# Optimization experiments

Hardware: AMD Instinct MI355X
Metric: run time of the kernel (lower is better)

Reference implementation:

```python
import jax, jax.numpy as jnp
import numpy as np

B, T, D_IN, D_H, D_OUT = 64, 512, 1024, 1024, 1024

def setup_inputs() -> dict:
    key = jax.random.key(0)
    k1, k2, k3 = jax.random.split(key, 3)
    scale_h = 1.0 / np.sqrt(D_IN + D_H)
    return {
        "input": jax.random.normal(k1, (B, T, D_IN), dtype=jnp.float32),
        "hidden": jnp.zeros((B, D_H), dtype=jnp.float32),
        "W_h": jax.random.normal(k2, (D_H, D_IN + D_H), dtype=jnp.float32) * scale_h,
        "b_h": jnp.zeros((D_H,), dtype=jnp.float32),
        "W_o": jax.random.normal(k3, (D_OUT, D_IN + D_H), dtype=jnp.float32) * scale_h,
        "b_o": jnp.zeros((D_OUT,), dtype=jnp.float32),
    }

def reference(input, hidden, W_h, b_h, W_o, b_o):
    # input: [B, T, D_in]; hidden: [B, D_h]
    # per step: combined = [x_t, h]; h' = combined @ W_h^T + b_h; o = combined @ W_o^T + b_o
    xs = jnp.swapaxes(input, 0, 1)  # [T, B, D_in]

    def step(h, x_t):
        combined = jnp.concatenate([x_t, h], axis=1)  # [B, D_in + D_h]
        h_new = combined @ W_h.T + b_h                # [B, D_h]
        o = combined @ W_o.T + b_o                    # [B, D_out]
        return h_new, o

    _, outs = jax.lax.scan(step, hidden, xs)          # outs: [T, B, D_out]
    return jnp.swapaxes(outs, 0, 1)                   # [B, T, D_out]
```

## Files before the change

### kernel.cpp

```cpp
#include <hip/hip_runtime.h>
#include <hip/hip_bf16.h>


typedef _Float16 f16;
typedef _Float16 f16x8 __attribute__((ext_vector_type(8)));
typedef _Float16 f16x4 __attribute__((ext_vector_type(4)));
typedef float f32x4 __attribute__((ext_vector_type(4)));
typedef int i32x4 __attribute__((ext_vector_type(4)));

#define T_LEN 512
#define BATCH 64
#define M_TOT (BATCH * T_LEN)


__global__ void k_prep_w(const float* __restrict__ Wh, const float* __restrict__ Wo,
                         f16* __restrict__ Wx, f16* __restrict__ Wr) {
    int n = blockIdx.x;
    int t4 = threadIdx.x * 4;
    const float* src = (n < 1024) ? (Wh + (size_t)n * 2048)
                                  : (Wo + (size_t)(n - 1024) * 2048);
    float4 a = *reinterpret_cast<const float4*>(src + t4);
    float4 b = *reinterpret_cast<const float4*>(src + 1024 + t4);
    f16x4 va, vb;
    va[0]=(f16)a.x; va[1]=(f16)a.y; va[2]=(f16)a.z; va[3]=(f16)a.w;
    vb[0]=(f16)b.x; vb[1]=(f16)b.y; vb[2]=(f16)b.z; vb[3]=(f16)b.w;
    *reinterpret_cast<f16x4*>(Wx + (size_t)n*1024 + t4) = va;
    *reinterpret_cast<f16x4*>(Wr + (size_t)n*1024 + t4) = vb;
}

__global__ void k_prep_x(const float* __restrict__ X, f16* __restrict__ Xf) {
    size_t i = ((size_t)blockIdx.x * 256 + threadIdx.x) * 8;
    float4 a = *reinterpret_cast<const float4*>(X + i);
    float4 b = *reinterpret_cast<const float4*>(X + i + 4);
    f16x8 v;
    v[0]=(f16)a.x; v[1]=(f16)a.y; v[2]=(f16)a.z; v[3]=(f16)a.w;
    v[4]=(f16)b.x; v[5]=(f16)b.y; v[6]=(f16)b.z; v[7]=(f16)b.w;
    *reinterpret_cast<f16x8*>(Xf + i) = v;
}

__global__ void k_init_h(const float* __restrict__ H0, f16* __restrict__ Hs) {
    int tid = blockIdx.x * 256 + threadIdx.x;
    int b = tid >> 7, kb = tid & 127;
    float4 x0 = *reinterpret_cast<const float4*>(H0 + (size_t)b*1024 + kb*8);
    float4 x1 = *reinterpret_cast<const float4*>(H0 + (size_t)b*1024 + kb*8 + 4);
    f16x8 v;
    v[0]=(f16)x0.x; v[1]=(f16)x0.y; v[2]=(f16)x0.z; v[3]=(f16)x0.w;
    v[4]=(f16)x1.x; v[5]=(f16)x1.y; v[6]=(f16)x1.z; v[7]=(f16)x1.w;
    size_t idx = (size_t)(b >> 4)*16384 + (size_t)kb*128 + (size_t)(b & 15)*8;
    *reinterpret_cast<f16x8*>(Hs + idx) = v;
}

__global__ void k_zero_flags(unsigned int* __restrict__ flags) {
    flags[blockIdx.x * 256 + threadIdx.x] = 0;
}

__global__ __launch_bounds__(256) void k_gemm1(
    const f16* __restrict__ Af, const f16* __restrict__ Bm,
    const float* __restrict__ bh, const float* __restrict__ bo,
    f16* __restrict__ Xh, float* __restrict__ Out)
{
    __shared__ f16 As[128*32];
    __shared__ f16 Bs[128*32];
    int m0 = blockIdx.x * 128;
    int n0 = blockIdx.y * 128;
    int t = threadIdx.x;
    int l = t & 63, w = t >> 6;
    int wm = w >> 1, wn = w & 1;
    int lm = l & 15, lh = l >> 4;

    f32x4 acc[4][4];
    #pragma unroll
    for (int i = 0; i < 4; i++)
        #pragma unroll
        for (int j = 0; j < 4; j++) acc[i][j] = (f32x4){0.f,0.f,0.f,0.f};

    const size_t lgo = (size_t)(l >> 2) * 2048 + (size_t)(l & 3) * 16;

    for (int kt = 0; kt < 32; ++kt) {
        __syncthreads();
        {
            const char* ga = (const char*)(Af + (size_t)(m0 + w*32) * 1024 + kt*32);
            const char* gb = (const char*)(Bm + (size_t)(n0 + w*32) * 1024 + kt*32);
            char* la = (char*)As + w * 2048;
            char* lb = (char*)Bs + w * 2048;
            #pragma unroll
            for (int j = 0; j < 2; ++j) {
                __builtin_amdgcn_global_load_lds(
                    (const __attribute__((address_space(1))) void*)(ga + (size_t)j*32768 + lgo),
                    (__attribute__((address_space(3))) void*)(la + j*1024), 16, 0, 0);
                __builtin_amdgcn_global_load_lds(
                    (const __attribute__((address_space(1))) void*)(gb + (size_t)j*32768 + lgo),
                    (__attribute__((address_space(3))) void*)(lb + j*1024), 16, 0, 0);
            }
        }
        asm volatile("s_waitcnt vmcnt(0)" ::: "memory");
        __syncthreads();

        f16x8 af[4], bf[4];
        #pragma unroll
        for (int i = 0; i < 4; i++)
            af[i] = *reinterpret_cast<const f16x8*>(As + (64*wm + 16*i + lm)*32 + 8*lh);
        #pragma unroll
        for (int j = 0; j < 4; j++)
            bf[j] = *reinterpret_cast<const f16x8*>(Bs + (64*wn + 16*j + lm)*32 + 8*lh);
        #pragma unroll
        for (int i = 0; i < 4; i++)
            #pragma unroll
            for (int j = 0; j < 4; j++)
                acc[i][j] = __builtin_amdgcn_mfma_f32_16x16x32_f16(af[i], bf[j], acc[i][j], 0, 0, 0);
    }

    int r0 = lh * 4;
    bool isH = (n0 < 1024);
    #pragma unroll
    for (int i = 0; i < 4; i++)
        #pragma unroll
        for (int j = 0; j < 4; j++) {
            int gmb = m0 + 64*wm + 16*i + r0;
            int gn  = n0 + 64*wn + 16*j + lm;
            #pragma unroll
            for (int r = 0; r < 4; r++) {
                float v = acc[i][j][r];
                int gm = gmb + r;
                if (isH) {
                    int tt = gm & 511, bb = gm >> 9;
                    size_t idx = (size_t)tt*65536 + (size_t)(bb>>4)*16384
                               + (size_t)(gn>>3)*128 + (size_t)(bb&15)*8 + (gn&7);
                    Xh[idx] = (f16)(v + bh[gn]);
                } else {
                    Out[(size_t)gm*1024 + (gn - 1024)] = v + bo[gn - 1024];
                }
            }
        }
}

__global__ __launch_bounds__(256) void k_sq(const f16* __restrict__ P, f16* __restrict__ Pout)
{
    __shared__ f16 As[128][40];
    __shared__ f16 Bs[128][40];
    int m0 = blockIdx.x * 128, n0 = blockIdx.y * 128;
    int t = threadIdx.x;
    int l = t & 63, wid = t >> 6;
    int wm = wid >> 1, wn = wid & 1;
    int lm = l & 15, lh = l >> 4;

    f32x4 acc[4][4];
    #pragma unroll
    for (int i = 0; i < 4; i++)
        #pragma unroll
        for (int j = 0; j < 4; j++) acc[i][j] = (f32x4){0.f,0.f,0.f,0.f};

    for (int kt = 0; kt < 32; ++kt) {
        __syncthreads();
        #pragma unroll
        for (int c = t; c < 512; c += 256) {
            int row = c >> 2, q = c & 3;
            *reinterpret_cast<float4*>(&As[row][q*8]) =
                *reinterpret_cast<const float4*>(P + (size_t)(m0+row)*1024 + kt*32 + q*8);
        }
        #pragma unroll
        for (int c = t; c < 512; c += 256) {
            int r = c >> 4, q = c & 15;
            f16x8 v = *reinterpret_cast<const f16x8*>(P + (size_t)(kt*32 + r)*1024 + n0 + q*8);
            #pragma unroll
            for (int e = 0; e < 8; ++e) Bs[q*8+e][r] = v[e];
        }
        __syncthreads();

        f16x8 af[4], bf[4];
        #pragma unroll
        for (int i = 0; i < 4; i++)
            af[i] = *reinterpret_cast<const f16x8*>(&As[64*wm + 16*i + lm][8*lh]);
        #pragma unroll
        for (int j = 0; j < 4; j++)
            bf[j] = *reinterpret_cast<const f16x8*>(&Bs[64*wn + 16*j + lm][8*lh]);
        #pragma unroll
        for (int i = 0; i < 4; i++)
            #pragma unroll
            for (int j = 0; j < 4; j++)
                acc[i][j] = __builtin_amdgcn_mfma_f32_16x16x32_f16(af[i], bf[j], acc[i][j], 0, 0, 0);
    }

    int r0 = lh * 4;
    #pragma unroll
    for (int i = 0; i < 4; i++)
        #pragma unroll
        for (int j = 0; j < 4; j++) {
            int gmb = m0 + 64*wm + 16*i + r0;
            int gn  = n0 + 64*wn + 16*j + lm;
            #pragma unroll
            for (int r = 0; r < 4; r++)
                Pout[(size_t)(gmb+r)*1024 + gn] = (f16)acc[i][j][r];
        }
}

__global__ __launch_bounds__(256) void k_vlevel(
    const f16* __restrict__ M, const f16* __restrict__ Src, f16* __restrict__ Dst,
    int srcOff, int srcStep, int dstOff, int dstStep)
{
    __shared__ f16 As[4096];
    __shared__ f16 Bs[128*32];
    int m0 = blockIdx.x * 128;
    int n0 = blockIdx.y * 128;
    int t = threadIdx.x;
    int l = t & 63, w = t >> 6;
    int wm = w >> 1, wn = w & 1;
    int lm = l & 15, lh = l >> 4;

    f32x4 acc[4][4];
    #pragma unroll
    for (int i = 0; i < 4; i++)
        #pragma unroll
        for (int j = 0; j < 4; j++) acc[i][j] = (f32x4){0.f,0.f,0.f,0.f};

    const size_t lgo = (size_t)(l >> 2) * 2048 + (size_t)(l & 3) * 16;
    const int kd0 = m0 >> 6;

    for (int kt = 0; kt < 32; ++kt) {
        __syncthreads();
        {
            #pragma unroll
            for (int j = 0; j < 2; ++j) {
                int ch  = w*2 + j;
                int kdl = ch >> 2, bgc = ch & 3;
                size_t slab = (size_t)(srcOff + srcStep * (2*(kd0 + kdl)));
                const char* gsrc = (const char*)(Src + slab*65536
                                    + (size_t)bgc*16384 + (size_t)kt*512) + (size_t)l*16;
                __builtin_amdgcn_global_load_lds(
                    (const __attribute__((address_space(1))) void*)gsrc,
                    (__attribute__((address_space(3))) void*)((char*)As + ch*1024), 16, 0, 0);
            }
            const char* gb = (const char*)(M + (size_t)(n0 + w*32) * 1024 + kt*32);
            char* lb = (char*)Bs + w * 2048;
            #pragma unroll
            for (int j = 0; j < 2; ++j)
                __builtin_amdgcn_global_load_lds(
                    (const __attribute__((address_space(1))) void*)(gb + (size_t)j*32768 + lgo),
                    (__attribute__((address_space(3))) void*)(lb + j*1024), 16, 0, 0);
        }
        asm volatile("s_waitcnt vmcnt(0)" ::: "memory");
        __syncthreads();

        f16x8 af[4], bf[4];
        #pragma unroll
        for (int i = 0; i < 4; i++)
            af[i] = *reinterpret_cast<const f16x8*>(As + wm*2048 + i*512 + lh*128 + lm*8);
        #pragma unroll
        for (int j = 0; j < 4; j++)
            bf[j] = *reinterpret_cast<const f16x8*>(Bs + (64*wn + 16*j + lm)*32 + 8*lh);
        #pragma unroll
        for (int i = 0; i < 4; i++)
            #pragma unroll
            for (int j = 0; j < 4; j++)
                acc[i][j] = __builtin_amdgcn_mfma_f32_16x16x32_f16(af[i], bf[j], acc[i][j], 0, 0, 0);
    }

    int r0 = lh * 4;
    #pragma unroll
    for (int i = 0; i < 4; i++)
        #pragma unroll
        for (int j = 0; j < 4; j++) {
            int gmb = m0 + 64*wm + 16*i + r0;
            int gn  = n0 + 64*wn + 16*j + lm;
            #pragma unroll
            for (int r = 0; r < 4; r++) {
                int gm = gmb + r;
                int kd = gm >> 6, bb = gm & 63;
                size_t pidx = (size_t)(bb>>4)*16384 + (size_t)(gn>>3)*128
                            + (size_t)(bb&15)*8 + (gn&7);
                size_t aslab = (size_t)(srcOff + srcStep * (2*kd + 1));
                float add = (float)Src[aslab*65536 + pidx];
                size_t dslab = (size_t)(dstOff + dstStep * kd);
                Dst[dslab*65536 + pidx] = (f16)(acc[i][j][r] + add);
            }
        }
}

__global__ void __launch_bounds__(256) __attribute__((amdgpu_waves_per_eu(1, 1)))
k_chain(
    const f16* __restrict__ W,
    const f16* __restrict__ U,
    f16* __restrict__ Hs,
    unsigned int* __restrict__ flags,
    int nstep, int mode, int nch)
{
    int wg = blockIdx.x;
    int r_ = wg & 7, s_ = wg >> 3;
    int g, cg, p, bg;
    if (mode == 1) { g = r_ >> 1; cg = ((r_ & 1) << 3) | s_; p = 0;       bg = g;     }
    else           { g = 2*r_ + (s_ >> 4); cg = s_ & 15;     p = g >> 2;  bg = g & 3; }
    int w  = threadIdx.x >> 6;
    int l  = threadIdx.x & 63;
    int lm = l & 15, lh = l >> 4;
    int ccol = cg * 64 + w * 16 + lm;

    __shared__ f16 hbuf[16384];
    __shared__ float lt[4][16][17];

    f16x8 bw[32];
    #pragma unroll
    for (int kt = 0; kt < 32; ++kt)
        bw[kt] = *reinterpret_cast<const f16x8*>(W + (size_t)ccol * 1024 + kt*32 + lh*8);
    #pragma unroll
    for (int kt = 0; kt < 32; ++kt)
        asm volatile("" : "+v"(bw[kt]));

    const int flagBase = g * 16;
    int b_ep = l & 15, cb_ep = l >> 4;

    for (int t = 0; t < nstep; ++t) {
        if (t > 0) {
            if (threadIdx.x < 16) {
                unsigned int tgt = (unsigned int)t;
                const unsigned int* fp = &flags[(flagBase + (int)threadIdx.x) * 8];
                while (__hip_atomic_load(fp, __ATOMIC_RELAXED, __HIP_MEMORY_SCOPE_AGENT) < tgt)
                    __builtin_amdgcn_s_sleep(1);
            }
            __syncthreads();
            asm volatile("" ::: "memory");
        }

        for (int i = 0; i < nch; ++i) {
            int c = p * nch + i;
            size_t rSlab, wSlab, uSlab;
            if (mode == 1) { rSlab = (size_t)(16*t); wSlab = rSlab + 16; uSlab = rSlab + 8; }
            else           { rSlab = (size_t)(c*16 + t); wSlab = rSlab + 1; uSlab = rSlab; }

            if (i > 0) __syncthreads();

            f16x8 xv;
            int cblk = cg*8 + w*2 + cb_ep;
            if (l < 32)
                xv = *reinterpret_cast<const f16x8*>(
                    U + uSlab*65536 + (size_t)bg*16384 + (size_t)cblk*128 + b_ep*8);

            {
                const char* gsrc = (const char*)Hs + (rSlab*65536 + (size_t)bg*16384)*2
                                 + (size_t)w*8192 + (size_t)l*16;
                char* ldst = (char*)hbuf + (size_t)w*8192;
                #pragma unroll
                for (int q = 0; q < 8; ++q)
                    __builtin_amdgcn_global_load_lds(
                        (const __attribute__((address_space(1))) void*)(gsrc + q*1024),
                        (__attribute__((address_space(3))) void*)(ldst + q*1024),
                        16, 0, 0);
            }
            asm volatile("s_waitcnt vmcnt(0)" ::: "memory");
            __syncthreads();

            f32x4 a0 = (f32x4){0.f,0.f,0.f,0.f};
            f32x4 a1 = (f32x4){0.f,0.f,0.f,0.f};
            #pragma unroll
            for (int kt = 0; kt < 32; ++kt) {
                f16x8 af = *reinterpret_cast<const f16x8*>(&hbuf[(size_t)(kt*4 + lh)*128 + lm*8]);
                if (kt & 1) a1 = __builtin_amdgcn_mfma_f32_16x16x32_f16(af, bw[kt], a1, 0, 0, 0);
                else        a0 = __builtin_amdgcn_mfma_f32_16x16x32_f16(af, bw[kt], a0, 0, 0, 0);
            }
            f32x4 acc = a0 + a1;

            #pragma unroll
            for (int r = 0; r < 4; ++r)
                lt[w][lh*4 + r][lm] = acc[r];

            if (l < 32) {
                f16x8 hv;
                #pragma unroll
                for (int e = 0; e < 8; ++e)
                    hv[e] = (f16)(lt[w][b_ep][cb_ep*8 + e] + (float)xv[e]);
                f16* dst = Hs + wSlab*65536 + (size_t)bg*16384 + (size_t)cblk*128 + b_ep*8;
                i32x4 iv = __builtin_bit_cast(i32x4, hv);
                asm volatile("global_store_dwordx4 %0, %1, off sc0 sc1"
                             :: "v"(dst), "v"(iv) : "memory");
            }
        }

        asm volatile("s_waitcnt vmcnt(0)" ::: "memory");
        __syncthreads();
        if (threadIdx.x == 0) {
            __builtin_amdgcn_fence(__ATOMIC_RELEASE, "agent");
            __hip_atomic_store(&flags[(flagBase + cg)*8], (unsigned int)(t+1),
                               __ATOMIC_RELAXED, __HIP_MEMORY_SCOPE_AGENT);
        }
    }
}

__global__ __launch_bounds__(256) void k_gemm2(
    const f16* __restrict__ Hs, const f16* __restrict__ Bm, float* __restrict__ Out)
{
    __shared__ f16 As[4096];
    __shared__ f16 Bs[128*32];
    int m0 = blockIdx.x * 128;
    int n0 = blockIdx.y * 128;
    int t = threadIdx.x;
    int l = t & 63, w = t >> 6;
    int wm = w >> 1, wn = w & 1;
    int lm = l & 15, lh = l >> 4;

    f32x4 acc[4][4];
    #pragma unroll
    for (int i = 0; i < 4; i++)
        #pragma unroll
        for (int j = 0; j < 4; j++) acc[i][j] = (f32x4){0.f,0.f,0.f,0.f};

    const size_t lgo = (size_t)(l >> 2) * 2048 + (size_t)(l & 3) * 16;
    const int tt0 = m0 >> 6;

    for (int kt = 0; kt < 32; ++kt) {
        __syncthreads();
        {
            #pragma unroll
            for (int j = 0; j < 2; ++j) {
                int ch  = w*2 + j;
                int ttl = ch >> 2, bgc = ch & 3;
                const char* gsrc = (const char*)(Hs + (size_t)(tt0 + ttl)*65536
                                    + (size_t)bgc*16384 + (size_t)kt*512) + (size_t)l*16;
                __builtin_amdgcn_global_load_lds(
                    (const __attribute__((address_space(1))) void*)gsrc,
                    (__attribute__((address_space(3))) void*)((char*)As + ch*1024), 16, 0, 0);
            }
            const char* gb = (const char*)(Bm + (size_t)(n0 + w*32) * 1024 + kt*32);
            char* lb = (char*)Bs + w * 2048;
            #pragma unroll
            for (int j = 0; j < 2; ++j)
                __builtin_amdgcn_global_load_lds(
                    (const __attribute__((address_space(1))) void*)(gb + (size_t)j*32768 + lgo),
                    (__attribute__((address_space(3))) void*)(lb + j*1024), 16, 0, 0);
        }
        asm volatile("s_waitcnt vmcnt(0)" ::: "memory");
        __syncthreads();

        f16x8 af[4], bf[4];
        #pragma unroll
        for (int i = 0; i < 4; i++)
            af[i] = *reinterpret_cast<const f16x8*>(As + wm*2048 + i*512 + lh*128 + lm*8);
        #pragma unroll
        for (int j = 0; j < 4; j++)
            bf[j] = *reinterpret_cast<const f16x8*>(Bs + (64*wn + 16*j + lm)*32 + 8*lh);
        #pragma unroll
        for (int i = 0; i < 4; i++)
            #pragma unroll
            for (int j = 0; j < 4; j++)
                acc[i][j] = __builtin_amdgcn_mfma_f32_16x16x32_f16(af[i], bf[j], acc[i][j], 0, 0, 0);
    }

    int r0 = lh * 4;
    #pragma unroll
    for (int i = 0; i < 4; i++)
        #pragma unroll
        for (int j = 0; j < 4; j++) {
            int gmb = m0 + 64*wm + 16*i + r0;
            int gn  = n0 + 64*wn + 16*j + lm;
            #pragma unroll
            for (int r = 0; r < 4; r++) {
                int gm = gmb + r;
                int bb = gm & 63, tt = gm >> 6;
                size_t o = ((size_t)bb*512 + tt)*1024 + gn;
                Out[o] += acc[i][j][r];
            }
        }
}


extern "C" void kernel_launch(void* const* d_in, const int* in_sizes, int n_in,
                              void* d_out, int out_size, void* d_ws, size_t ws_size,
                              hipStream_t stream) {
    const float* X  = (const float*)d_in[0];
    const float* H0 = (const float*)d_in[1];
    const float* Wh = (const float*)d_in[2];
    const float* bh = (const float*)d_in[3];
    const float* Wo = (const float*)d_in[4];
    const float* bo = (const float*)d_in[5];
    float* Out = (float*)d_out;

    char* ws = (char*)d_ws;
    f16* Wx = (f16*)(ws);
    f16* Pa = (f16*)(ws);
    f16* Pb = (f16*)(ws + (size_t)2*1024*1024);
    f16* Wr = (f16*)(ws + (size_t)4*1024*1024);
    f16* Xh = (f16*)(ws + (size_t)8*1024*1024);
    f16* Hs = (f16*)(ws + (size_t)8*1024*1024 + (size_t)M_TOT*1024*2);
    f16* Xf = Hs;
    unsigned int* flags = (unsigned int*)(ws + (size_t)8*1024*1024 + (size_t)2*M_TOT*1024*2);

    hipLaunchKernelGGL(k_prep_w, dim3(2048), dim3(256), 0, stream, Wh, Wo, Wx, Wr);
    hipLaunchKernelGGL(k_prep_x, dim3(16384), dim3(256), 0, stream, X, Xf);
    hipLaunchKernelGGL(k_gemm1, dim3(256, 16), dim3(256), 0, stream, Xf, Wx, bh, bo, Xh, Out);
    hipLaunchKernelGGL(k_init_h, dim3(32), dim3(256), 0, stream, H0, Hs);

    hipLaunchKernelGGL(k_sq, dim3(8,8), dim3(256), 0, stream, Wr, Pa);
    hipLaunchKernelGGL(k_vlevel, dim3(128,8), dim3(256), 0, stream, Wr, Xh, Hs, 0,1, 1,1);
    hipLaunchKernelGGL(k_vlevel, dim3(64,8),  dim3(256), 0, stream, Pa, Hs, Hs, 1,1, 257,2);
    hipLaunchKernelGGL(k_sq, dim3(8,8), dim3(256), 0, stream, Pa, Pb);
    hipLaunchKernelGGL(k_vlevel, dim3(32,8),  dim3(256), 0, stream, Pb, Hs, Hs, 257,2, 2,4);
    hipLaunchKernelGGL(k_sq, dim3(8,8), dim3(256), 0, stream, Pb, Pa);
    hipLaunchKernelGGL(k_vlevel, dim3(16,8),  dim3(256), 0, stream, Pa, Hs, Hs, 2,4, 8,16);
    hipLaunchKernelGGL(k_sq, dim3(8,8), dim3(256), 0, stream, Pa, Pb);

    hipLaunchKernelGGL(k_zero_flags, dim3(8), dim3(256), 0, stream, flags);
    {
        int nstep = 31, mode = 1, nch = 1;
        void* args[] = { (void*)&Pb, (void*)&Hs, (void*)&Hs, (void*)&flags,
                         (void*)&nstep, (void*)&mode, (void*)&nch };
        if (hipLaunchCooperativeKernel((const void*)k_chain, dim3(64), dim3(256),
                                       args, 0, stream) != hipSuccess) {
            hipLaunchKernelGGL(k_chain, dim3(64), dim3(256), 0, stream,
                               Pb, Hs, Hs, flags, 31, 1, 1);
        }
    }

    hipLaunchKernelGGL(k_zero_flags, dim3(8), dim3(256), 0, stream, flags);
    {
        int nstep = 15, mode = 2, nch = 8;
        void* args[] = { (void*)&Wr, (void*)&Xh, (void*)&Hs, (void*)&flags,
                         (void*)&nstep, (void*)&mode, (void*)&nch };
        if (hipLaunchCooperativeKernel((const void*)k_chain, dim3(256), dim3(256),
                                       args, 0, stream) != hipSuccess) {
            hipLaunchKernelGGL(k_chain, dim3(256), dim3(256), 0, stream,
                               Wr, Xh, Hs, flags, 15, 2, 8);
        }
    }

    f16* Wro = Wr + (size_t)1024*1024;
    hipLaunchKernelGGL(k_gemm2, dim3(256, 8), dim3(256), 0, stream, Hs, Wro, Out);
}
```

Measured before the change: 1.107 ms.

## Double-buffer hidden-state staging in chain kernel and widen gemm1 K tile

The recurrent chain kernel now keeps two LDS buffers for the hidden state and issues the async global-to-LDS load for the next chunk before computing the current one. It waits only on the older loads via a partial vmcnt, so load latency overlaps the MFMA work. Separately, gemm1 stages 64-wide K tiles instead of 32, halving its loop iterations and barriers. The costs are double the LDS for hbuf, an extra barrier per chunk, and a vmcnt count that is hand-tuned and fragile. Mode 1 (nch=1 likely) sees no overlap.

```diff
diff --git a/kernel.cpp b/kernel.cpp
--- a/kernel.cpp
+++ b/kernel.cpp
@@ -59,8 +59,8 @@
     const float* __restrict__ bh, const float* __restrict__ bo,
     f16* __restrict__ Xh, float* __restrict__ Out)
 {
-    __shared__ f16 As[128*32];
-    __shared__ f16 Bs[128*32];
+    __shared__ f16 As[128*64];
+    __shared__ f16 Bs[128*64];
     int m0 = blockIdx.x * 128;
     int n0 = blockIdx.y * 128;
     int t = threadIdx.x;
@@ -74,40 +74,43 @@
         #pragma unroll
         for (int j = 0; j < 4; j++) acc[i][j] = (f32x4){0.f,0.f,0.f,0.f};
 
-    const size_t lgo = (size_t)(l >> 2) * 2048 + (size_t)(l & 3) * 16;
-
-    for (int kt = 0; kt < 32; ++kt) {
+    const size_t lgo = (size_t)(l >> 3) * 2048 + (size_t)(l & 7) * 16;
+
+    for (int kt = 0; kt < 16; ++kt) {
         __syncthreads();
         {
-            const char* ga = (const char*)(Af + (size_t)(m0 + w*32) * 1024 + kt*32);
-            const char* gb = (const char*)(Bm + (size_t)(n0 + w*32) * 1024 + kt*32);
-            char* la = (char*)As + w * 2048;
-            char* lb = (char*)Bs + w * 2048;
-            #pragma unroll
-            for (int j = 0; j < 2; ++j) {
-                __builtin_amdgcn_global_load_lds(
-                    (const __attribute__((address_space(1))) void*)(ga + (size_t)j*32768 + lgo),
+            const char* ga = (const char*)(Af + (size_t)(m0 + w*32) * 1024 + kt*64);
+            const char* gb = (const char*)(Bm + (size_t)(n0 + w*32) * 1024 + kt*64);
+            char* la = (char*)As + w * 4096;
+            char* lb = (char*)Bs + w * 4096;
+            #pragma unroll
+            for (int j = 0; j < 4; ++j) {
+                __builtin_amdgcn_global_load_lds(
+                    (const __attribute__((address_space(1))) void*)(ga + (size_t)j*16384 + lgo),
                     (__attribute__((address_space(3))) void*)(la + j*1024), 16, 0, 0);
                 __builtin_amdgcn_global_load_lds(
-                    (const __attribute__((address_space(1))) void*)(gb + (size_t)j*32768 + lgo),
+                    (const __attribute__((address_space(1))) void*)(gb + (size_t)j*16384 + lgo),
                     (__attribute__((address_space(3))) void*)(lb + j*1024), 16, 0, 0);
             }
         }
         asm volatile("s_waitcnt vmcnt(0)" ::: "memory");
         __syncthreads();
 
-        f16x8 af[4], bf[4];
-        #pragma unroll
-        for (int i = 0; i < 4; i++)
-            af[i] = *reinterpret_cast<const f16x8*>(As + (64*wm + 16*i + lm)*32 + 8*lh);
-        #pragma unroll
-        for (int j = 0; j < 4; j++)
-            bf[j] = *reinterpret_cast<const f16x8*>(Bs + (64*wn + 16*j + lm)*32 + 8*lh);
-        #pragma unroll
-        for (int i = 0; i < 4; i++)
+        #pragma unroll
+        for (int kh = 0; kh < 2; ++kh) {
+            f16x8 af[4], bf[4];
+            #pragma unroll
+            for (int i = 0; i < 4; i++)
+                af[i] = *reinterpret_cast<const f16x8*>(As + (64*wm + 16*i + lm)*64 + kh*32 + 8*lh);
             #pragma unroll
             for (int j = 0; j < 4; j++)
-                acc[i][j] = __builtin_amdgcn_mfma_f32_16x16x32_f16(af[i], bf[j], acc[i][j], 0, 0, 0);
+                bf[j] = *reinterpret_cast<const f16x8*>(Bs + (64*wn + 16*j + lm)*64 + kh*32 + 8*lh);
+            #pragma unroll
+            for (int i = 0; i < 4; i++)
+                #pragma unroll
+                for (int j = 0; j < 4; j++)
+                    acc[i][j] = __builtin_amdgcn_mfma_f32_16x16x32_f16(af[i], bf[j], acc[i][j], 0, 0, 0);
+        }
     }
 
     int r0 = lh * 4;
@@ -294,7 +297,7 @@
     int lm = l & 15, lh = l >> 4;
     int ccol = cg * 64 + w * 16 + lm;
 
-    __shared__ f16 hbuf[16384];
+    __shared__ f16 hbuf[2][16384];
     __shared__ float lt[4][16][17];
 
     f16x8 bw[32];
@@ -307,6 +310,7 @@
 
     const int flagBase = g * 16;
     int b_ep = l & 15, cb_ep = l >> 4;
+    int cblk = cg*8 + w*2 + cb_ep;
 
     for (int t = 0; t < nstep; ++t) {
         if (t > 0) {
@@ -320,39 +324,54 @@
             asm volatile("" ::: "memory");
         }
 
+        auto slabs = [&](int i, size_t& rS, size_t& wS, size_t& uS) {
+            if (mode == 1) { rS = (size_t)(16*t); wS = rS + 16; uS = rS + 8; }
+            else { int c = p*nch + i; rS = (size_t)(c*16 + t); wS = rS + 1; uS = rS; }
+        };
+        auto STAGE = [&](size_t rS, int buf) {
+            const char* gsrc = (const char*)Hs + (rS*65536 + (size_t)bg*16384)*2
+                             + (size_t)w*8192 + (size_t)l*16;
+            char* ldst = (char*)&hbuf[buf][0] + (size_t)w*8192;
+            #pragma unroll
+            for (int q = 0; q < 8; ++q)
+                __builtin_amdgcn_global_load_lds(
+                    (const __attribute__((address_space(1))) void*)(gsrc + q*1024),
+                    (__attribute__((address_space(3))) void*)(ldst + q*1024),
+                    16, 0, 0);
+        };
+        auto XV = [&](size_t uS) -> f16x8 {
+            f16x8 v = {};
+            if (l < 32)
+                v = *reinterpret_cast<const f16x8*>(
+                    U + uS*65536 + (size_t)bg*16384 + (size_t)cblk*128 + b_ep*8);
+            return v;
+        };
+
+        f16x8 xv0, xv1;
+        {
+            size_t rS, wS, uS; slabs(0, rS, wS, uS);
+            STAGE(rS, 0);
+            xv0 = XV(uS);
+        }
+
         for (int i = 0; i < nch; ++i) {
-            int c = p * nch + i;
-            size_t rSlab, wSlab, uSlab;
-            if (mode == 1) { rSlab = (size_t)(16*t); wSlab = rSlab + 16; uSlab = rSlab + 8; }
-            else           { rSlab = (size_t)(c*16 + t); wSlab = rSlab + 1; uSlab = rSlab; }
-
-            if (i > 0) __syncthreads();
-
-            f16x8 xv;
-            int cblk = cg*8 + w*2 + cb_ep;
-            if (l < 32)
-                xv = *reinterpret_cast<const f16x8*>(
-                    U + uSlab*65536 + (size_t)bg*16384 + (size_t)cblk*128 + b_ep*8);
-
-            {
-                const char* gsrc = (const char*)Hs + (rSlab*65536 + (size_t)bg*16384)*2
-                                 + (size_t)w*8192 + (size_t)l*16;
-                char* ldst = (char*)hbuf + (size_t)w*8192;
-                #pragma unroll
-                for (int q = 0; q < 8; ++q)
-                    __builtin_amdgcn_global_load_lds(
-                        (const __attribute__((address_space(1))) void*)(gsrc + q*1024),
-                        (__attribute__((address_space(3))) void*)(ldst + q*1024),
-                        16, 0, 0);
-            }
-            asm volatile("s_waitcnt vmcnt(0)" ::: "memory");
+            int nxt = i + 1;
+            if (nxt < nch) {
+                size_t rS, wS, uS; slabs(nxt, rS, wS, uS);
+                STAGE(rS, nxt & 1);
+                if (nxt & 1) xv1 = XV(uS); else xv0 = XV(uS);
+                asm volatile("s_waitcnt vmcnt(9)" ::: "memory");
+            } else {
+                asm volatile("s_waitcnt vmcnt(0)" ::: "memory");
+            }
             __syncthreads();
 
+            const f16* cbuf = &hbuf[i & 1][0];
             f32x4 a0 = (f32x4){0.f,0.f,0.f,0.f};
             f32x4 a1 = (f32x4){0.f,0.f,0.f,0.f};
             #pragma unroll
             for (int kt = 0; kt < 32; ++kt) {
-                f16x8 af = *reinterpret_cast<const f16x8*>(&hbuf[(size_t)(kt*4 + lh)*128 + lm*8]);
+                f16x8 af = *reinterpret_cast<const f16x8*>(&cbuf[(size_t)(kt*4 + lh)*128 + lm*8]);
                 if (kt & 1) a1 = __builtin_amdgcn_mfma_f32_16x16x32_f16(af, bw[kt], a1, 0, 0, 0);
                 else        a0 = __builtin_amdgcn_mfma_f32_16x16x32_f16(af, bw[kt], a0, 0, 0, 0);
             }
@@ -363,15 +382,18 @@
                 lt[w][lh*4 + r][lm] = acc[r];
 
             if (l < 32) {
+                f16x8 xvc = (i & 1) ? xv1 : xv0;
+                size_t rS, wS, uS; slabs(i, rS, wS, uS);
                 f16x8 hv;
                 #pragma unroll
                 for (int e = 0; e < 8; ++e)
-                    hv[e] = (f16)(lt[w][b_ep][cb_ep*8 + e] + (float)xv[e]);
-                f16* dst = Hs + wSlab*65536 + (size_t)bg*16384 + (size_t)cblk*128 + b_ep*8;
+                    hv[e] = (f16)(lt[w][b_ep][cb_ep*8 + e] + (float)xvc[e]);
+                f16* dst = Hs + wS*65536 + (size_t)bg*16384 + (size_t)cblk*128 + b_ep*8;
                 i32x4 iv = __builtin_bit_cast(i32x4, hv);
                 asm volatile("global_store_dwordx4 %0, %1, off sc0 sc1"
                              :: "v"(dst), "v"(iv) : "memory");
             }
+            __syncthreads();
         }
 
         asm volatile("s_waitcnt vmcnt(0)" ::: "memory");
```

Result: slower. 1.130 ms (+2.2%).
